# Performance work log

Measured on AMD Instinct MI355X. Metric: run time of the kernel, lower is better.

Reference implementation:

```python
import jax, jax.numpy as jnp
import numpy as np

B, L, CIN, COUT, HEADS = 8, 2048, 256, 256, 4
HD = COUT // HEADS
NEG_SLOPE = 0.2


def setup_inputs() -> dict:
    key = jax.random.key(0)
    k1, k2, k3, k4, k5 = jax.random.split(key, 5)
    x = jax.random.normal(k1, (B, L, CIN), dtype=jnp.float32)
    adj_mask = jax.random.randint(k2, (B, L, L), 0, 2) > 0  # bool [B,L,L]
    W = jax.random.normal(k3, (COUT, CIN), dtype=jnp.float32) * (1.0 / np.sqrt(CIN))
    att_src = jax.random.normal(k4, (1, HEADS, 1, HD), dtype=jnp.float32) * 0.1
    att_dst = jax.random.normal(k5, (1, HEADS, 1, HD), dtype=jnp.float32) * 0.1
    return {"x": x, "adj_mask": adj_mask, "W": W, "att_src": att_src, "att_dst": att_dst}


def reference(x, adj_mask, W, att_src, att_dst):
    Bb, Ll, _ = x.shape
    # linear projection (no bias), split heads: [B, H, L, D]
    h = jnp.einsum('blc,oc->blo', x, W).reshape(Bb, Ll, HEADS, HD).transpose(0, 2, 1, 3)
    # additive GAT scores
    a_src = jnp.sum(h * att_src, axis=-1, keepdims=True)          # [B,H,L,1]
    a_dst = jnp.sum(h * att_dst, axis=-1, keepdims=True)          # [B,H,L,1]
    e = a_src + jnp.swapaxes(a_dst, 2, 3)                          # [B,H,L,L]
    e = jnp.where(e >= 0, e, NEG_SLOPE * e)                        # leaky relu
    fill = jnp.finfo(e.dtype).min
    e = jnp.where(adj_mask[:, None, :, :], e, fill)                # mask non-edges
    alpha = jax.nn.softmax(e, axis=-1)                             # [B,H,L,L]
    # dropout is identity in eval/reference mode
    out = jnp.einsum('bhij,bhjd->bhid', alpha, h)                  # [B,H,L,D]
    return out.transpose(0, 2, 1, 3).reshape(Bb, Ll, COUT)
```

## Files before the change

### kernel.cpp

```cpp
#include <hip/hip_runtime.h>

#define B_ 8
#define L_ 2048
#define CIN_ 256
#define COUT_ 256
#define HEADS_ 4
#define HD_ 64
#define NEG_SLOPE_ 0.2f
#define LOG2E_ 1.4426950408889634f

#define TI 32
#define TJ 64
#define NJT (L_ / TJ)

typedef __attribute__((ext_vector_type(4))) float f32x4;
typedef __attribute__((ext_vector_type(8))) __bf16 bf16x8;
typedef __attribute__((ext_vector_type(4))) __bf16 bf16x4;


__global__ __launch_bounds__(256, 4)
void pack_kernel(const int* __restrict__ adj, unsigned long long* __restrict__ abitsT) {
  const size_t wid = ((size_t)blockIdx.x * 256 + threadIdx.x) >> 6;
  const int lane = threadIdx.x & 63;
  const int* p = adj + wid * 256 + lane;
  unsigned long long b0 = __ballot(p[0]   != 0);
  unsigned long long b1 = __ballot(p[64]  != 0);
  unsigned long long b2 = __ballot(p[128] != 0);
  unsigned long long b3 = __ballot(p[192] != 0);
  if (lane == 0) {
    const size_t row = wid >> 3;
    const int jw0 = (int)(wid & 7) * 4;
    const size_t bb = row >> 11, l = row & 2047;
    unsigned long long* dst = abitsT + (bb << 16) + l;
    dst[(size_t)(jw0 + 0) << 11] = b0;
    dst[(size_t)(jw0 + 1) << 11] = b1;
    dst[(size_t)(jw0 + 2) << 11] = b2;
    dst[(size_t)(jw0 + 3) << 11] = b3;
  }
}

__global__ __launch_bounds__(256, 2)
void proj_kernel(const float* __restrict__ x, const float* __restrict__ W,
                 const float* __restrict__ att_src, const float* __restrict__ att_dst,
                 __bf16* __restrict__ hF, float* __restrict__ a_src,
                 float* __restrict__ a_dst) {
  __shared__ __align__(16) __bf16 Wl[COUT_][80];
  __shared__ __align__(16) __bf16 Al[2][2][512];

  const int tid = threadIdx.x;
  const int r0 = blockIdx.x * TI;
  const int b  = r0 >> 11;
  const int l0 = r0 & (L_ - 1);

  const int w = tid >> 6, lane = tid & 63, col = lane & 15, q = lane >> 4;
  const int si = tid >> 3, soct = tid & 7;
  const int wn = tid >> 2, wkq = tid & 3;

  f32x4 acc[2][4];
#pragma unroll
  for (int mt = 0; mt < 2; ++mt)
#pragma unroll
    for (int nt = 0; nt < 4; ++nt) acc[mt][nt] = (f32x4)0.f;

  for (int kc = 0; kc < CIN_ / 64; ++kc) {
    __syncthreads();
#pragma unroll
    for (int rg = 0; rg < 4; ++rg) {
      const int row = rg * 64 + wn;
      const float4* ws = (const float4*)(W + (size_t)row * CIN_ + kc * 64 + wkq * 16);
#pragma unroll
      for (int u = 0; u < 4; ++u) {
        float4 f = ws[u];
        bf16x4 v;
        v[0] = (__bf16)f.x; v[1] = (__bf16)f.y; v[2] = (__bf16)f.z; v[3] = (__bf16)f.w;
        *(bf16x4*)&Wl[row][wkq * 16 + u * 4] = v;
      }
    }
    {
      const float4* xs = (const float4*)(x + (size_t)(r0 + si) * CIN_ + kc * 64 + soct * 8);
      float4 f0 = xs[0], f1 = xs[1];
      bf16x8 v;
      v[0] = (__bf16)f0.x; v[1] = (__bf16)f0.y; v[2] = (__bf16)f0.z; v[3] = (__bf16)f0.w;
      v[4] = (__bf16)f1.x; v[5] = (__bf16)f1.y; v[6] = (__bf16)f1.z; v[7] = (__bf16)f1.w;
      *(bf16x8*)&Al[si >> 4][soct >> 2][(((soct & 3) << 4) + (si & 15)) << 3] = v;
    }
    __syncthreads();

    bf16x8 af[2][2], bfr[2][4];
#pragma unroll
    for (int mt = 0; mt < 2; ++mt)
#pragma unroll
      for (int kt = 0; kt < 2; ++kt)
        af[mt][kt] = *(const bf16x8*)&Al[mt][kt][lane << 3];
#pragma unroll
    for (int kt = 0; kt < 2; ++kt)
#pragma unroll
      for (int nt = 0; nt < 4; ++nt)
        bfr[kt][nt] = *(const bf16x8*)&Wl[w * 64 + nt * 16 + col][kt * 32 + q * 8];
#pragma unroll
    for (int kt = 0; kt < 2; ++kt)
#pragma unroll
      for (int mt = 0; mt < 2; ++mt)
#pragma unroll
        for (int nt = 0; nt < 4; ++nt)
          acc[mt][nt] = __builtin_amdgcn_mfma_f32_16x16x32_bf16(
              af[mt][kt], bfr[kt][nt], acc[mt][nt], 0, 0, 0);
  }

  float asv[4], adv[4];
#pragma unroll
  for (int nt = 0; nt < 4; ++nt) {
    asv[nt] = att_src[w * 64 + nt * 16 + col];
    adv[nt] = att_dst[w * 64 + nt * 16 + col];
  }
#pragma unroll
  for (int mt = 0; mt < 2; ++mt)
#pragma unroll
    for (int reg = 0; reg < 4; ++reg) {
      float s = 0.f, d = 0.f;
#pragma unroll
      for (int nt = 0; nt < 4; ++nt) {
        s = fmaf(acc[mt][nt][reg], asv[nt], s);
        d = fmaf(acc[mt][nt][reg], adv[nt], d);
      }
      s += __shfl_xor(s, 1, 64); d += __shfl_xor(d, 1, 64);
      s += __shfl_xor(s, 2, 64); d += __shfl_xor(d, 2, 64);
      s += __shfl_xor(s, 4, 64); d += __shfl_xor(d, 4, 64);
      s += __shfl_xor(s, 8, 64); d += __shfl_xor(d, 8, 64);
      if (col == 0) {
        int il = mt * 16 + q * 4 + reg;
        a_src[((size_t)(b * HEADS_ + w) << 11) + l0 + il] = s * LOG2E_;
        a_dst[((size_t)(b * HEADS_ + w) << 11) + l0 + il] = d * LOG2E_;
      }
    }

  {
    const int jt_p = l0 >> 6;
    const int kt_p = (l0 >> 5) & 1;
    const int qhi = q >> 1, qlo = q & 1;
#pragma unroll
    for (int mt = 0; mt < 2; ++mt) {
      const int qp = mt * 2 + qhi;
#pragma unroll
      for (int nt = 0; nt < 4; ++nt) {
        bf16x4 v;
        v[0] = (__bf16)acc[mt][nt][0];
        v[1] = (__bf16)acc[mt][nt][1];
        v[2] = (__bf16)acc[mt][nt][2];
        v[3] = (__bf16)acc[mt][nt][3];
        const size_t off =
            ((((size_t)(b * HEADS_ + w) * 32 + jt_p) * 2 + kt_p) * 4 + nt) * 512 +
            (qp * 16 + col) * 8 + qlo * 4;
        *(bf16x4*)(hF + off) = v;
      }
    }
  }
}

__global__ __launch_bounds__(256, 2)
void attn_kernel(const __bf16* __restrict__ hF, const float* __restrict__ a_src,
                 const float* __restrict__ a_dst,
                 const unsigned long long* __restrict__ abitsT,
                 float* __restrict__ out) {
  const int tid = threadIdx.x;
  const int b  = blockIdx.x & 7;
  const int i0 = (blockIdx.x >> 3) * 32;

  const int w = tid >> 6, lane = tid & 63, col = lane & 15, q = lane >> 4;

  const size_t hl = (size_t)(b * HEADS_ + w);
  const float asr[2] = {a_src[(hl << 11) + i0 + col],
                        a_src[(hl << 11) + i0 + 16 + col]};
  const float* adb = a_dst + (hl << 11) + q * 8;
  const __bf16* hb = hF + hl * 131072 + lane * 8;
  const unsigned long long* mb = abitsT + ((size_t)b << 16) + i0 + col;

  bf16x8 bones;
#pragma unroll
  for (int e = 0; e < 8; ++e) bones[e] = (__bf16)1.0f;

  f32x4 acc[2][4], accl[2];
#pragma unroll
  for (int mt = 0; mt < 2; ++mt) {
    accl[mt] = (f32x4)0.f;
#pragma unroll
    for (int nt = 0; nt < 4; ++nt) acc[mt][nt] = (f32x4)0.f;
  }

  unsigned long long cm0 = mb[0], cm1 = mb[16];
  float4 cd[2][2];
#pragma unroll
  for (int kt = 0; kt < 2; ++kt) {
    cd[kt][0] = *(const float4*)(adb + kt * 32);
    cd[kt][1] = *(const float4*)(adb + kt * 32 + 4);
  }

  for (int jt = 0; jt < NJT; ++jt) {
    bf16x8 cb[2][4];
#pragma unroll
    for (int kt = 0; kt < 2; ++kt)
#pragma unroll
      for (int nt = 0; nt < 4; ++nt)
        cb[kt][nt] = *(const bf16x8*)(hb + jt * 4096 + (kt * 4 + nt) * 512);

    const int jn = (jt < NJT - 1) ? jt + 1 : jt;
    const unsigned long long nm0 = mb[(size_t)jn << 11];
    const unsigned long long nm1 = mb[((size_t)jn << 11) + 16];
    float4 nd[2][2];
#pragma unroll
    for (int kt = 0; kt < 2; ++kt) {
      nd[kt][0] = *(const float4*)(adb + jn * 64 + kt * 32);
      nd[kt][1] = *(const float4*)(adb + jn * 64 + kt * 32 + 4);
    }

    bf16x8 av[2][2];
#pragma unroll
    for (int mt = 0; mt < 2; ++mt) {
      const unsigned long long bw = mt ? cm1 : cm0;
#pragma unroll
      for (int kt = 0; kt < 2; ++kt) {
        const unsigned int tsh = ((unsigned int)(bw >> (kt * 32))) >> (q * 8);
        const float dd[8] = {cd[kt][0].x, cd[kt][0].y, cd[kt][0].z, cd[kt][0].w,
                             cd[kt][1].x, cd[kt][1].y, cd[kt][1].z, cd[kt][1].w};
#pragma unroll
        for (int e = 0; e < 8; ++e) {
          float t = asr[mt] + dd[e];
          t = fmaxf(t, NEG_SLOPE_ * t);
          float p = ((tsh >> e) & 1u) ? __builtin_exp2f(t) : 0.f;
          av[mt][kt][e] = (__bf16)p;
        }
      }
    }

#pragma unroll
    for (int kt = 0; kt < 2; ++kt)
#pragma unroll
      for (int mt = 0; mt < 2; ++mt) {
#pragma unroll
        for (int nt = 0; nt < 4; ++nt)
          acc[mt][nt] = __builtin_amdgcn_mfma_f32_16x16x32_bf16(
              av[mt][kt], cb[kt][nt], acc[mt][nt], 0, 0, 0);
        accl[mt] = __builtin_amdgcn_mfma_f32_16x16x32_bf16(
            av[mt][kt], bones, accl[mt], 0, 0, 0);
      }

    cm0 = nm0; cm1 = nm1;
#pragma unroll
    for (int kt = 0; kt < 2; ++kt) {
      cd[kt][0] = nd[kt][0];
      cd[kt][1] = nd[kt][1];
    }
  }

#pragma unroll
  for (int mt = 0; mt < 2; ++mt)
#pragma unroll
    for (int reg = 0; reg < 4; ++reg) {
      const int m = q * 4 + reg;
      const float linv = 1.0f / accl[mt][reg];
      const size_t orow =
          ((size_t)(b * L_ + i0 + mt * 16 + m)) * COUT_ + w * 64;
#pragma unroll
      for (int nt = 0; nt < 4; ++nt)
        out[orow + nt * 16 + col] = acc[mt][nt][reg] * linv;
    }
}

extern "C" void kernel_launch(void* const* d_in, const int* in_sizes, int n_in,
                              void* d_out, int out_size, void* d_ws, size_t ws_size,
                              hipStream_t stream) {
  const float* x       = (const float*)d_in[0];
  const int*   adj     = (const int*)d_in[1];
  const float* W       = (const float*)d_in[2];
  const float* att_src = (const float*)d_in[3];
  const float* att_dst = (const float*)d_in[4];
  float* out = (float*)d_out;

  char* ws = (char*)d_ws;
  __bf16* hF = (__bf16*)ws;
  float* a_src = (float*)(ws + (8u << 20));
  float* a_dst = (float*)(ws + (8u << 20) + (256u << 10));
  unsigned long long* abitsT =
      (unsigned long long*)(ws + (8u << 20) + (512u << 10));

  pack_kernel<<<(B_ * L_ * (L_ / 256)) / 4, 256, 0, stream>>>(adj, abitsT);
  proj_kernel<<<(B_ * L_) / TI, 256, 0, stream>>>(x, W, att_src, att_dst, hF, a_src, a_dst);
  attn_kernel<<<B_ * (L_ / 32), 256, 0, stream>>>(hF, a_src, a_dst, abitsT, out);
}
```

Before: 290.7 us.

## Factor exp of leaky-relu scores into precomputed per-node exponentials

Uses exp(leaky(a+b)) = max(exp(a)exp(b), exp(0.2a)exp(0.2b)) to precompute four exponentials per node in the projection kernel. The attention inner loop then does two multiplies and a max instead of an add, a leaky relu and an exp2 per score, which removes transcendental work from the hot loop. It doubles the per-node score data read in the loop and drops the one-tile-ahead prefetch of those values. It also carries overflow risk because there is no max subtraction, and products of large exponentials may overflow fp32.

```diff
diff --git a/kernel.cpp b/kernel.cpp
--- a/kernel.cpp
+++ b/kernel.cpp
@@ -42,8 +42,8 @@
 __global__ __launch_bounds__(256, 2)
 void proj_kernel(const float* __restrict__ x, const float* __restrict__ W,
                  const float* __restrict__ att_src, const float* __restrict__ att_dst,
-                 __bf16* __restrict__ hF, float* __restrict__ a_src,
-                 float* __restrict__ a_dst) {
+                 __bf16* __restrict__ hF, float2* __restrict__ aE,
+                 float2* __restrict__ aF) {
   __shared__ __align__(16) __bf16 Wl[COUT_][80];
   __shared__ __align__(16) __bf16 Al[2][2][512];
 
@@ -129,8 +129,14 @@
       s += __shfl_xor(s, 8, 64); d += __shfl_xor(d, 8, 64);
       if (col == 0) {
         int il = mt * 16 + q * 4 + reg;
-        a_src[((size_t)(b * HEADS_ + w) << 11) + l0 + il] = s * LOG2E_;
-        a_dst[((size_t)(b * HEADS_ + w) << 11) + l0 + il] = d * LOG2E_;
+        const size_t idx = ((size_t)(b * HEADS_ + w) << 11) + l0 + il;
+        float2 ev, fv;
+        ev.x = __builtin_exp2f(s * LOG2E_);
+        ev.y = __builtin_exp2f(s * (LOG2E_ * NEG_SLOPE_));
+        fv.x = __builtin_exp2f(d * LOG2E_);
+        fv.y = __builtin_exp2f(d * (LOG2E_ * NEG_SLOPE_));
+        aE[idx] = ev;
+        aF[idx] = fv;
       }
     }
 
@@ -158,8 +164,8 @@
 }
 
 __global__ __launch_bounds__(256, 2)
-void attn_kernel(const __bf16* __restrict__ hF, const float* __restrict__ a_src,
-                 const float* __restrict__ a_dst,
+void attn_kernel(const __bf16* __restrict__ hF, const float2* __restrict__ aE,
+                 const float2* __restrict__ aF,
                  const unsigned long long* __restrict__ abitsT,
                  float* __restrict__ out) {
   const int tid = threadIdx.x;
@@ -169,9 +175,9 @@
   const int w = tid >> 6, lane = tid & 63, col = lane & 15, q = lane >> 4;
 
   const size_t hl = (size_t)(b * HEADS_ + w);
-  const float asr[2] = {a_src[(hl << 11) + i0 + col],
-                        a_src[(hl << 11) + i0 + 16 + col]};
-  const float* adb = a_dst + (hl << 11) + q * 8;
+  const float2 EE[2] = {aE[(hl << 11) + i0 + col],
+                        aE[(hl << 11) + i0 + 16 + col]};
+  const float* afb = (const float*)(aF + (hl << 11)) + q * 16;
   const __bf16* hb = hF + hl * 131072 + lane * 8;
   const unsigned long long* mb = abitsT + ((size_t)b << 16) + i0 + col;
 
@@ -188,12 +194,6 @@
   }
 
   unsigned long long cm0 = mb[0], cm1 = mb[16];
-  float4 cd[2][2];
-#pragma unroll
-  for (int kt = 0; kt < 2; ++kt) {
-    cd[kt][0] = *(const float4*)(adb + kt * 32);
-    cd[kt][1] = *(const float4*)(adb + kt * 32 + 4);
-  }
 
   for (int jt = 0; jt < NJT; ++jt) {
     bf16x8 cb[2][4];
@@ -202,31 +202,32 @@
 #pragma unroll
       for (int nt = 0; nt < 4; ++nt)
         cb[kt][nt] = *(const bf16x8*)(hb + jt * 4096 + (kt * 4 + nt) * 512);
+    float cf[2][16];
+#pragma unroll
+    for (int kt = 0; kt < 2; ++kt)
+#pragma unroll
+      for (int u = 0; u < 4; ++u)
+        *(float4*)&cf[kt][u * 4] =
+            *(const float4*)(afb + jt * 128 + kt * 64 + u * 4);
 
     const int jn = (jt < NJT - 1) ? jt + 1 : jt;
     const unsigned long long nm0 = mb[(size_t)jn << 11];
     const unsigned long long nm1 = mb[((size_t)jn << 11) + 16];
-    float4 nd[2][2];
-#pragma unroll
-    for (int kt = 0; kt < 2; ++kt) {
-      nd[kt][0] = *(const float4*)(adb + jn * 64 + kt * 32);
-      nd[kt][1] = *(const float4*)(adb + jn * 64 + kt * 32 + 4);
-    }
 
     bf16x8 av[2][2];
 #pragma unroll
     for (int mt = 0; mt < 2; ++mt) {
       const unsigned long long bw = mt ? cm1 : cm0;
+      const float Ex = EE[mt].x, Ey = EE[mt].y;
 #pragma unroll
       for (int kt = 0; kt < 2; ++kt) {
         const unsigned int tsh = ((unsigned int)(bw >> (kt * 32))) >> (q * 8);
-        const float dd[8] = {cd[kt][0].x, cd[kt][0].y, cd[kt][0].z, cd[kt][0].w,
-                             cd[kt][1].x, cd[kt][1].y, cd[kt][1].z, cd[kt][1].w};
 #pragma unroll
         for (int e = 0; e < 8; ++e) {
-          float t = asr[mt] + dd[e];
-          t = fmaxf(t, NEG_SLOPE_ * t);
-          float p = ((tsh >> e) & 1u) ? __builtin_exp2f(t) : 0.f;
+          const float m1 = Ex * cf[kt][2 * e];
+          const float m2 = Ey * cf[kt][2 * e + 1];
+          const float pm = fmaxf(m1, m2);
+          const float p = (tsh & (1u << e)) ? pm : 0.f;
           av[mt][kt][e] = (__bf16)p;
         }
       }
@@ -245,11 +246,6 @@
       }
 
     cm0 = nm0; cm1 = nm1;
-#pragma unroll
-    for (int kt = 0; kt < 2; ++kt) {
-      cd[kt][0] = nd[kt][0];
-      cd[kt][1] = nd[kt][1];
-    }
   }
 
 #pragma unroll
@@ -278,12 +274,12 @@
 
   char* ws = (char*)d_ws;
   __bf16* hF = (__bf16*)ws;
-  float* a_src = (float*)(ws + (8u << 20));
-  float* a_dst = (float*)(ws + (8u << 20) + (256u << 10));
+  float2* aE = (float2*)(ws + (8u << 20));
+  float2* aF = (float2*)(ws + (9u << 20));
   unsigned long long* abitsT =
-      (unsigned long long*)(ws + (8u << 20) + (512u << 10));
+      (unsigned long long*)(ws + (10u << 20));
 
   pack_kernel<<<(B_ * L_ * (L_ / 256)) / 4, 256, 0, stream>>>(adj, abitsT);
-  proj_kernel<<<(B_ * L_) / TI, 256, 0, stream>>>(x, W, att_src, att_dst, hF, a_src, a_dst);
-  attn_kernel<<<B_ * (L_ / 32), 256, 0, stream>>>(hF, a_src, a_dst, abitsT, out);
-}
+  proj_kernel<<<(B_ * L_) / TI, 256, 0, stream>>>(x, W, att_src, att_dst, hF, aE, aF);
+  attn_kernel<<<B_ * (L_ / 32), 256, 0, stream>>>(hF, aE, aF, abitsT, out);
+}
```

New measurement: 265.3 us. 1.1x faster.
